# Kernel optimization log

Hardware: AMD Instinct MI355X
Metric: run time of the kernel (lower is better)

The kernel has to match this reference:

```python
import jax, jax.numpy as jnp
import numpy as np

N_NODES = 100000
N_EDGES = 1600000
N_GRAPHS = 512
HID = 192
EPS = 1e-5


def setup_inputs() -> dict:
    key = jax.random.key(0)
    ks = jax.random.split(key, 16)
    x = jax.random.normal(ks[0], (N_NODES, 1), dtype=jnp.float32)
    edge_index = jax.random.randint(ks[1], (2, N_EDGES), 0, N_NODES, dtype=jnp.int64)
    batch = jnp.sort(jax.random.randint(ks[2], (N_NODES,), 0, N_GRAPHS, dtype=jnp.int64))
    def lin(k, fi, fo):
        # torch nn.Linear default init: U(-1/sqrt(fi), 1/sqrt(fi))
        b = 1.0 / np.sqrt(fi)
        return jax.random.uniform(k, (fi, fo), jnp.float32, -b, b)
    return {
        "x": x, "edge_index": edge_index, "batch": batch,
        "W1": lin(ks[3], 1, HID), "b1": jnp.zeros((HID,), jnp.float32),
        "g1": jnp.ones((HID,), jnp.float32), "be1": jnp.zeros((HID,), jnp.float32), "a1": jnp.ones((HID,), jnp.float32),
        "W2": lin(ks[4], HID, HID), "b2": jnp.zeros((HID,), jnp.float32),
        "g2": jnp.ones((HID,), jnp.float32), "be2": jnp.zeros((HID,), jnp.float32), "a2": jnp.ones((HID,), jnp.float32),
        "Wc1": lin(ks[5], HID, HID // 2), "bc1": jax.random.uniform(ks[6], (HID // 2,), jnp.float32, -1/np.sqrt(HID), 1/np.sqrt(HID)),
        "Wc2": lin(ks[7], HID // 2, 4), "bc2": jax.random.uniform(ks[8], (4,), jnp.float32, -1/np.sqrt(HID // 2), 1/np.sqrt(HID // 2)),
    }


def gcn_conv(x, W, b, row, col, n):
    # PyG GCNConv: h = xW; add self-loops; norm = d^-1/2[src] * d^-1/2[dst]; scatter-add to dst; + bias
    h = x @ W
    sl = jnp.arange(n, dtype=row.dtype)
    r = jnp.concatenate([row, sl])
    c = jnp.concatenate([col, sl])
    deg = jax.ops.segment_sum(jnp.ones_like(c, dtype=h.dtype), c, num_segments=n)
    dinv = jnp.where(deg > 0, jax.lax.rsqrt(deg), 0.0)
    norm = dinv[r] * dinv[c]                      # [E+N]
    msg = h[r] * norm[:, None]                    # [E+N, HID] dominant gather
    return jax.ops.segment_sum(msg, c, num_segments=n) + b


def graph_norm(x, batch, gamma, beta, alpha, g):
    cnt = jax.ops.segment_sum(jnp.ones((x.shape[0],), x.dtype), batch, num_segments=g)
    cnt = jnp.maximum(cnt, 1.0)[:, None]
    mean = jax.ops.segment_sum(x, batch, num_segments=g) / cnt
    out = x - alpha * mean[batch]
    var = jax.ops.segment_sum(out * out, batch, num_segments=g) / cnt
    out = out * jax.lax.rsqrt(var + EPS)[batch]
    return gamma * out + beta


def reference(x, edge_index, batch, W1, b1, g1, be1, a1, W2, b2, g2, be2, a2, Wc1, bc1, Wc2, bc2):
    n = x.shape[0]
    row, col = edge_index[0], edge_index[1]
    h = gcn_conv(x, W1, b1, row, col, n)
    h = jax.nn.relu(graph_norm(h, batch, g1, be1, a1, N_GRAPHS))
    h = gcn_conv(h, W2, b2, row, col, n)
    h = jax.nn.relu(graph_norm(h, batch, g2, be2, a2, N_GRAPHS))
    # global mean pool (dropout is identity in eval mode)
    cnt = jnp.maximum(jax.ops.segment_sum(jnp.ones((n,), h.dtype), batch, num_segments=N_GRAPHS), 1.0)
    pooled = jax.ops.segment_sum(h, batch, num_segments=N_GRAPHS) / cnt[:, None]
    z = jax.nn.relu(pooled @ Wc1 + bc1)
    return z @ Wc2 + bc2
```

## Files before the change

### kernel.cpp

```cpp
#include <hip/hip_runtime.h>
#include <hip/hip_bf16.h>
#include <hip/hip_fp16.h>

#define N_NODES 100000
#define N_PAD 100032
#define N_EDGES 1600000
#define N_GRAPHS 512
#define HID 192
#define EPSV 1e-5f

using f16x8 = __attribute__((ext_vector_type(8))) _Float16;
using f16x4 = __attribute__((ext_vector_type(4))) _Float16;
using f32x4 = __attribute__((ext_vector_type(4))) float;

__global__ void k_count(const int* __restrict__ col, int* __restrict__ cnt) {
    int e = blockIdx.x * blockDim.x + threadIdx.x;
    if (e < N_EDGES) atomicAdd(&cnt[col[e]], 1);
}

__global__ void k_misc(const float* __restrict__ W2, _Float16* __restrict__ W2h,
                       const int* __restrict__ batch, int* __restrict__ gstart) {
    int id = blockIdx.x * blockDim.x + threadIdx.x;
    if (id < HID * HID) W2h[id] = (_Float16)W2[id];
    int g = id - HID * HID;
    if (g >= 0 && g <= N_GRAPHS) {
        if (g == N_GRAPHS) { gstart[g] = N_NODES; return; }
        int lo = 0, hi = N_NODES;
        while (lo < hi) { int mid = (lo + hi) >> 1; if (batch[mid] < g) lo = mid + 1; else hi = mid; }
        gstart[g] = lo;
    }
}

__global__ void k_scan_partial(const int* __restrict__ cnt, int* __restrict__ bsum) {
    __shared__ int sd[256];
    int base = blockIdx.x * 1024;
    int t = threadIdx.x;
    int s = 0;
    for (int j = 0; j < 4; ++j) {
        int i = base + j * 256 + t;
        if (i < N_NODES) s += cnt[i];
    }
    sd[t] = s; __syncthreads();
    for (int off = 128; off > 0; off >>= 1) {
        if (t < off) sd[t] += sd[t + off];
        __syncthreads();
    }
    if (t == 0) bsum[blockIdx.x] = sd[0];
}

__global__ void k_scan_final(const int* __restrict__ cnt, const int* __restrict__ bsum,
                             int nb, int* __restrict__ row_ptr, int* __restrict__ cursor,
                             float* __restrict__ dinv, const float* __restrict__ x,
                             float* __restrict__ xp) {
    __shared__ int sd[256];
    __shared__ int s_off;
    int bid = blockIdx.x;
    int t = threadIdx.x;
    int part = 0;
    for (int i = t; i < bid; i += 256) part += bsum[i];
    sd[t] = part; __syncthreads();
    for (int off = 128; off > 0; off >>= 1) {
        if (t < off) sd[t] += sd[t + off];
        __syncthreads();
    }
    if (t == 0) s_off = sd[0];
    __syncthreads();
    int base = bid * 1024;
    int idx0 = base + t * 4;
    int c[4]; int tot = 0;
    for (int j = 0; j < 4; ++j) {
        int i = idx0 + j;
        c[j] = (i < N_NODES) ? cnt[i] : 0;
        tot += c[j];
    }
    sd[t] = tot; __syncthreads();
    for (int off = 1; off < 256; off <<= 1) {
        int v = (t >= off) ? sd[t - off] : 0;
        __syncthreads();
        sd[t] += v;
        __syncthreads();
    }
    int excl = sd[t] - tot + s_off;
    for (int j = 0; j < 4; ++j) {
        int i = idx0 + j;
        if (i < N_NODES) {
            row_ptr[i] = excl;
            cursor[i] = excl;
            float dv = rsqrtf((float)(c[j] + 1));
            dinv[i] = dv;
            xp[i] = x[i] * dv;
            excl += c[j];
        }
    }
    if (bid == nb - 1 && t == 255) row_ptr[N_NODES] = excl;
}

#define FILL_WIN 8
#define FILL_RANGE (N_NODES / FILL_WIN)
#define EPR ((N_EDGES + 255) / 256)
__global__ void __launch_bounds__(256) k_fill(const int* __restrict__ row,
                                              const int* __restrict__ col,
                                              int* __restrict__ cursor,
                                              int* __restrict__ csr_src) {
    int w = blockIdx.x & 7;
    int rank = blockIdx.x >> 3;
    int lo = w * FILL_RANGE;
    int hi = (w == FILL_WIN - 1) ? N_NODES : lo + FILL_RANGE;
    int e0 = rank * EPR;
    int e1 = min(e0 + EPR, N_EDGES);
    for (int e = e0 + threadIdx.x; e < e1; e += 256) {
        int c = col[e];
        if (c >= lo && c < hi) {
            int pos = atomicAdd(&cursor[c], 1);
            csr_src[pos] = row[e];
        }
    }
}

__global__ void k_layer1(const float* __restrict__ x, const float* __restrict__ xp,
                         const int* __restrict__ batch,
                         const int* __restrict__ row_ptr, const int* __restrict__ csr_src,
                         const float* __restrict__ dinv, float4* __restrict__ node_info) {
    int v = blockIdx.x * blockDim.x + threadIdx.x;
    if (v >= N_NODES) return;
    int e0 = row_ptr[v], e1 = row_ptr[v + 1];
    float acc = 0.f;
    for (int base = e0; base < e1; base += 16) {
        int src[16]; float xv[16];
#pragma unroll
        for (int j = 0; j < 16; ++j) { int e = base + j; src[j] = csr_src[(e < e1) ? e : e0]; }
#pragma unroll
        for (int j = 0; j < 16; ++j) { xv[j] = xp[src[j]]; }
#pragma unroll
        for (int j = 0; j < 16; ++j) { acc += (base + j < e1) ? xv[j] : 0.f; }
    }
    float dv = dinv[v];
    float u = dv * acc + x[v] * dv * dv;
    node_info[v] = make_float4(u, dv, __int_as_float((int)batch[v]), 0.f);
}

__global__ void __launch_bounds__(192) k_stats_ab(const float4* __restrict__ node_info,
                                                  const int* __restrict__ gstart,
                                                  const float* __restrict__ W1, const float* __restrict__ b1,
                                                  const float* __restrict__ g1, const float* __restrict__ be1,
                                                  const float* __restrict__ a1,
                                                  float* __restrict__ A, float* __restrict__ B) {
    __shared__ float sd[192], sd2[192];
    int g = blockIdx.x, t = threadIdx.x;
    int i0 = gstart[g], i1 = gstart[g + 1];
    float s = 0.f, s2 = 0.f;
    for (int i = i0 + t; i < i1; i += 192) { float u = node_info[i].x; s += u; s2 += u * u; }
    sd[t] = s; sd2[t] = s2; __syncthreads();
    for (int off = 96; off >= 3; off >>= 1) {
        if (t < off) { sd[t] += sd[t + off]; sd2[t] += sd2[t + off]; }
        __syncthreads();
    }
    float sum_u = sd[0] + sd[1] + sd[2];
    float sum_u2 = sd2[0] + sd2[1] + sd2[2];
    float cntf = fmaxf((float)(i1 - i0), 1.f);
    float m = sum_u / cntf;
    float es2 = sum_u2 / cntf;
    int f = t;
    float w = W1[f], bb = b1[f], al = a1[f];
    float c2 = bb * (1.f - al);
    float d = al * m;
    float eud2 = es2 - 2.f * d * m + d * d;
    float var = w * w * eud2 + 2.f * w * c2 * (m - d) + c2 * c2;
    float rs = rsqrtf(var + EPSV);
    float gam = g1[f];
    A[g * HID + f] = gam * rs * w;
    B[g * HID + f] = gam * rs * (c2 - w * d) + be1[f];
}

__global__ void __launch_bounds__(256) k_x1(const float4* __restrict__ node_info,
                                            const float* __restrict__ A,
                                            const float* __restrict__ B,
                                            _Float16* __restrict__ X1p) {
    int wid = threadIdx.x >> 6;
    int lane = threadIdx.x & 63;
    int v = blockIdx.x * 4 + wid;
    if (v >= N_NODES) return;
    float4 ni = node_info[v];
    float u = ni.x, dv = ni.y;
    int g = __float_as_int(ni.z);
    int c4 = (lane < 48 ? lane : 47) * 4;
    float4 Av = *(const float4*)(A + g * HID + c4);
    float4 Bv = *(const float4*)(B + g * HID + c4);
    f16x4 o;
    o[0] = (_Float16)(fmaxf(fmaf(Av.x, u, Bv.x), 0.f) * dv);
    o[1] = (_Float16)(fmaxf(fmaf(Av.y, u, Bv.y), 0.f) * dv);
    o[2] = (_Float16)(fmaxf(fmaf(Av.z, u, Bv.z), 0.f) * dv);
    o[3] = (_Float16)(fmaxf(fmaf(Av.w, u, Bv.w), 0.f) * dv);
    if (lane < 48) *(f16x4*)(X1p + (size_t)v * HID + c4) = o;
}

#define CH 8
__global__ void __launch_bounds__(256) k_conv2(const _Float16* __restrict__ X1p,
                                               const float* __restrict__ dinv,
                                               const int* __restrict__ row_ptr,
                                               const int* __restrict__ csr_src,
                                               _Float16* __restrict__ aggh) {
    int wid = threadIdx.x >> 6;
    int lane = threadIdx.x & 63;
    int v = blockIdx.x * 4 + wid;
    if (v >= N_NODES) return;
    unsigned c8 = (unsigned)(lane < 48 ? lane : 47) * 8u;
    const char* Xb = (const char*)X1p;
    float dv = dinv[v];
    f16x4 sv = *(const f16x4*)(Xb + (unsigned)v * (HID * 2) + c8);
    float a0 = (float)sv[0], a1 = (float)sv[1], a2 = (float)sv[2], a3 = (float)sv[3];
    int e0 = row_ptr[v], e1 = row_ptr[v + 1];
    for (int b = e0; b < e1; b += CH) {
        unsigned off[CH]; float wgt[CH];
#pragma unroll
        for (int j = 0; j < CH; ++j) {
            int e = b + j;
            off[j] = (unsigned)csr_src[(e < e1) ? e : e0] * (unsigned)(HID * 2) + c8;
            wgt[j] = (e < e1) ? 1.f : 0.f;
        }
        f16x4 rv[CH];
#pragma unroll
        for (int j = 0; j < CH; ++j)
            rv[j] = *(const f16x4*)(Xb + off[j]);
#pragma unroll
        for (int j = 0; j < CH; ++j) {
            a0 = fmaf(wgt[j], (float)rv[j][0], a0);
            a1 = fmaf(wgt[j], (float)rv[j][1], a1);
            a2 = fmaf(wgt[j], (float)rv[j][2], a2);
            a3 = fmaf(wgt[j], (float)rv[j][3], a3);
        }
    }
    if (lane < 48) {
        f16x4 o;
        o[0] = (_Float16)(a0 * dv);
        o[1] = (_Float16)(a1 * dv);
        o[2] = (_Float16)(a2 * dv);
        o[3] = (_Float16)(a3 * dv);
        *(f16x4*)((char*)aggh + (unsigned)v * (HID * 2) + c8) = o;
    }
}

#define BM 64
__global__ void __launch_bounds__(256) k_gemm(const _Float16* __restrict__ A,
                                              const _Float16* __restrict__ W,
                                              const float* __restrict__ b2,
                                              const int* __restrict__ batch,
                                              _Float16* __restrict__ H,
                                              float* __restrict__ sums,
                                              float* __restrict__ sumsq) {
    __shared__ _Float16 a_lds[BM * HID];
    __shared__ int bb[BM];
    int t = threadIdx.x;
    int wid = t >> 6, lane = t & 63;
    int row0 = blockIdx.x * BM;
    if (t < BM) { int gr = row0 + t; bb[t] = (gr < N_NODES) ? batch[gr] : -1; }
    const char* Ablk = (const char*)(A + (size_t)row0 * HID);
#pragma unroll
    for (int it = 0; it < 6; ++it) {
        int bo = (it * 256 + t) * 16;
        int r = bo / 384;
        int swz = bo ^ ((r & 7) << 4);
        *(float4*)((char*)a_lds + swz) = *(const float4*)(Ablk + bo);
    }
    int n0 = wid * 48;
    int bn = n0 + (lane & 15);
    int bk0 = (lane >> 4) << 3;
    f16x8 bfr[6][3];
#pragma unroll
    for (int kc = 0; kc < 6; ++kc)
#pragma unroll
        for (int nt = 0; nt < 3; ++nt) {
            const _Float16* src = W + (size_t)(kc * 32 + bk0) * HID + bn + nt * 16;
            f16x8 v;
#pragma unroll
            for (int j = 0; j < 8; ++j) v[j] = src[(size_t)j * HID];
            bfr[kc][nt] = v;
        }
    __syncthreads();
    f32x4 acc[4][3];
#pragma unroll
    for (int mt = 0; mt < 4; ++mt)
#pragma unroll
        for (int nt = 0; nt < 3; ++nt) acc[mt][nt] = (f32x4){0.f, 0.f, 0.f, 0.f};
    int ar = lane & 15;
#pragma unroll
    for (int mt = 0; mt < 4; ++mt) {
        int r = mt * 16 + ar;
        int rbase = r * 384;
        int sw = (r & 7) << 4;
#pragma unroll
        for (int kc = 0; kc < 6; ++kc) {
            int bo = (rbase + (kc * 32 + bk0) * 2) ^ sw;
            f16x8 a = *(const f16x8*)((const char*)a_lds + bo);
            acc[mt][0] = __builtin_amdgcn_mfma_f32_16x16x32_f16(a, bfr[kc][0], acc[mt][0], 0, 0, 0);
            acc[mt][1] = __builtin_amdgcn_mfma_f32_16x16x32_f16(a, bfr[kc][1], acc[mt][1], 0, 0, 0);
            acc[mt][2] = __builtin_amdgcn_mfma_f32_16x16x32_f16(a, bfr[kc][2], acc[mt][2], 0, 0, 0);
        }
    }
    int cn = lane & 15;
    int rb = (lane >> 4) * 4;
    float bias[3];
#pragma unroll
    for (int nt = 0; nt < 3; ++nt) bias[nt] = b2[n0 + nt * 16 + cn];
    int gA = bb[0];
    int lastv = min(BM, N_NODES - row0) - 1;
    int gB = bb[lastv];
    float sA[3] = {0.f,0.f,0.f}, qA[3] = {0.f,0.f,0.f};
    float sB[3] = {0.f,0.f,0.f}, qB[3] = {0.f,0.f,0.f};
#pragma unroll
    for (int mt = 0; mt < 4; ++mt)
#pragma unroll
        for (int r = 0; r < 4; ++r) {
            int ridx = mt * 16 + rb + r;
            int grow = row0 + ridx;
            if (grow < N_NODES) {
                int gi = bb[ridx];
                _Float16* o = H + (size_t)grow * HID;
#pragma unroll
                for (int nt = 0; nt < 3; ++nt) {
                    float val = acc[mt][nt][r] + bias[nt];
                    o[n0 + nt * 16 + cn] = (_Float16)val;
                    if (gi == gA) { sA[nt] += val; qA[nt] += val * val; }
                    else          { sB[nt] += val; qB[nt] += val * val; }
                }
            }
        }
#pragma unroll
    for (int nt = 0; nt < 3; ++nt) {
        sA[nt] += __shfl_xor(sA[nt], 16); sA[nt] += __shfl_xor(sA[nt], 32);
        qA[nt] += __shfl_xor(qA[nt], 16); qA[nt] += __shfl_xor(qA[nt], 32);
        sB[nt] += __shfl_xor(sB[nt], 16); sB[nt] += __shfl_xor(sB[nt], 32);
        qB[nt] += __shfl_xor(qB[nt], 16); qB[nt] += __shfl_xor(qB[nt], 32);
    }
    if (lane < 16) {
#pragma unroll
        for (int nt = 0; nt < 3; ++nt) {
            int colf = n0 + nt * 16 + cn;
            atomicAdd(&sums[gA * HID + colf], sA[nt]);
            atomicAdd(&sumsq[gA * HID + colf], qA[nt]);
            if (gB != gA) {
                atomicAdd(&sums[gB * HID + colf], sB[nt]);
                atomicAdd(&sumsq[gB * HID + colf], qB[nt]);
            }
        }
    }
}

__global__ void __launch_bounds__(192) k_pool(const _Float16* __restrict__ h,
                                              const int* __restrict__ batch,
                                              const int* __restrict__ gstart,
                                              const float* __restrict__ sums,
                                              const float* __restrict__ sumsq,
                                              const float* __restrict__ g2,
                                              const float* __restrict__ be2,
                                              const float* __restrict__ a2,
                                              float* __restrict__ pooled) {
    int f = threadIdx.x;
    int r0 = blockIdx.x * 64;
    int r1 = min(r0 + 64, N_NODES);
    float al = a2[f], gam = g2[f], bet = be2[f];
    int g = batch[r0];
    float Cg, Dg;
    auto cd = [&](int gg) {
        float cntf = fmaxf((float)(gstart[gg + 1] - gstart[gg]), 1.f);
        float mh = sums[gg * HID + f] / cntf;
        float msq = sumsq[gg * HID + f] / cntf;
        float var = msq - 2.f * al * mh * mh + al * al * mh * mh;
        Cg = gam * rsqrtf(var + EPSV);
        Dg = bet - Cg * al * mh;
    };
    cd(g);
    float s = 0.f;
    int i = r0;
    for (; i + 4 <= r1; i += 4) {
        int g0 = batch[i], g3 = batch[i + 3];
        float v0 = (float)h[(size_t)(i + 0) * HID + f];
        float v1 = (float)h[(size_t)(i + 1) * HID + f];
        float v2 = (float)h[(size_t)(i + 2) * HID + f];
        float v3 = (float)h[(size_t)(i + 3) * HID + f];
        if (g0 == g && g3 == g) {
            s += fmaxf(fmaf(Cg, v0, Dg), 0.f) + fmaxf(fmaf(Cg, v1, Dg), 0.f);
            s += fmaxf(fmaf(Cg, v2, Dg), 0.f) + fmaxf(fmaf(Cg, v3, Dg), 0.f);
        } else {
            float vv[4] = {v0, v1, v2, v3};
            for (int j = 0; j < 4; ++j) {
                int gi = batch[i + j];
                if (gi != g) {
                    atomicAdd(&pooled[g * HID + f], s);
                    s = 0.f; g = gi; cd(g);
                }
                s += fmaxf(fmaf(Cg, vv[j], Dg), 0.f);
            }
        }
    }
    for (; i < r1; ++i) {
        int gi = batch[i];
        float v = (float)h[(size_t)i * HID + f];
        if (gi != g) {
            atomicAdd(&pooled[g * HID + f], s);
            s = 0.f; g = gi; cd(g);
        }
        s += fmaxf(fmaf(Cg, v, Dg), 0.f);
    }
    atomicAdd(&pooled[g * HID + f], s);
}

__global__ void __launch_bounds__(128) k_mlp(const float* __restrict__ pooled,
                                             const int* __restrict__ gstart,
                                             const float* __restrict__ Wc1,
                                             const float* __restrict__ bc1,
                                             const float* __restrict__ Wc2,
                                             const float* __restrict__ bc2,
                                             float* __restrict__ out) {
    __shared__ float p[HID];
    __shared__ float z[96];
    int g = blockIdx.x, t = threadIdx.x;
    float inv = 1.f / fmaxf((float)(gstart[g + 1] - gstart[g]), 1.f);
    for (int i = t; i < HID; i += 128) p[i] = pooled[g * HID + i] * inv;
    __syncthreads();
    if (t < 96) {
        float acc = bc1[t];
        for (int k = 0; k < HID; ++k) acc += p[k] * Wc1[k * 96 + t];
        z[t] = fmaxf(acc, 0.f);
    }
    __syncthreads();
    if (t < 4) {
        float acc = bc2[t];
        for (int j = 0; j < 96; ++j) acc += z[j] * Wc2[j * 4 + t];
        out[g * 4 + t] = acc;
    }
}

extern "C" void kernel_launch(void* const* d_in, const int* in_sizes, int n_in,
                              void* d_out, int out_size, void* d_ws, size_t ws_size,
                              hipStream_t stream) {
    const float* x   = (const float*)d_in[0];
    const int* eidx  = (const int*)d_in[1];
    const int* batch = (const int*)d_in[2];
    const float* W1  = (const float*)d_in[3];
    const float* b1  = (const float*)d_in[4];
    const float* g1  = (const float*)d_in[5];
    const float* be1 = (const float*)d_in[6];
    const float* a1  = (const float*)d_in[7];
    const float* W2  = (const float*)d_in[8];
    const float* b2  = (const float*)d_in[9];
    const float* g2  = (const float*)d_in[10];
    const float* be2 = (const float*)d_in[11];
    const float* a2  = (const float*)d_in[12];
    const float* Wc1 = (const float*)d_in[13];
    const float* bc1 = (const float*)d_in[14];
    const float* Wc2 = (const float*)d_in[15];
    const float* bc2 = (const float*)d_in[16];
    const int* row = eidx;
    const int* col = eidx + N_EDGES;
    float* out = (float*)d_out;

    char* ws = (char*)d_ws;
    size_t off = 0;
    auto alloc = [&](size_t bytes) -> char* {
        char* p = ws + off;
        off = (off + bytes + 255) & ~(size_t)255;
        return p;
    };
    int*   cnt     = (int*)  alloc(N_NODES * 4);
    float* sums2   = (float*)alloc(N_GRAPHS * HID * 4);
    float* sumsq2  = (float*)alloc(N_GRAPHS * HID * 4);
    float* pooled  = (float*)alloc(N_GRAPHS * HID * 4);
    size_t zbytes  = off;
    int*   bsum    = (int*)  alloc(128 * 4);
    int*   row_ptr = (int*)  alloc((N_NODES + 1) * 4);
    int*   cursor  = (int*)  alloc(N_NODES * 4);
    int*   csr_src = (int*)  alloc(N_EDGES * 4);
    float* dinv    = (float*)alloc(N_NODES * 4);
    float* xp      = (float*)alloc(N_NODES * 4);
    float4* node_info = (float4*)alloc((size_t)N_NODES * 16);
    float* Atab    = (float*)alloc(N_GRAPHS * HID * 4);
    float* Btab    = (float*)alloc(N_GRAPHS * HID * 4);
    int*   gstart  = (int*)  alloc((N_GRAPHS + 1) * 4);
    _Float16* X1p  = (_Float16*)alloc((size_t)N_NODES * HID * 2);
    _Float16* aggh = (_Float16*)alloc((size_t)N_PAD * HID * 2);
    _Float16* h2   = (_Float16*)alloc((size_t)N_NODES * HID * 2);
    _Float16* W2h  = (_Float16*)alloc((size_t)HID * HID * 2);

    hipMemsetAsync(ws, 0, zbytes, stream);
    k_misc<<<(HID * HID + N_GRAPHS + 1 + 255) / 256, 256, 0, stream>>>(W2, W2h, batch, gstart);
    k_count<<<(N_EDGES + 255) / 256, 256, 0, stream>>>(col, cnt);
    int PB = (N_NODES + 1023) / 1024;
    k_scan_partial<<<PB, 256, 0, stream>>>(cnt, bsum);
    k_scan_final<<<PB, 256, 0, stream>>>(cnt, bsum, PB, row_ptr, cursor, dinv, x, xp);
    k_fill<<<2048, 256, 0, stream>>>(row, col, cursor, csr_src);
    k_layer1<<<(N_NODES + 255) / 256, 256, 0, stream>>>(x, xp, batch, row_ptr, csr_src, dinv, node_info);
    k_stats_ab<<<N_GRAPHS, 192, 0, stream>>>(node_info, gstart, W1, b1, g1, be1, a1, Atab, Btab);
    k_x1<<<(N_NODES + 3) / 4, 256, 0, stream>>>(node_info, Atab, Btab, X1p);
    k_conv2<<<(N_NODES + 3) / 4, 256, 0, stream>>>(X1p, dinv, row_ptr, csr_src, aggh);
    k_gemm<<<(N_NODES + BM - 1) / BM, 256, 0, stream>>>(aggh, W2h, b2, batch, h2, sums2, sumsq2);
    int SB = (N_NODES + 63) / 64;
    k_pool<<<SB, 192, 0, stream>>>(h2, batch, gstart, sums2, sumsq2, g2, be2, a2, pooled);
    k_mlp<<<N_GRAPHS, 128, 0, stream>>>(pooled, gstart, Wc1, bc1, Wc2, bc2, out);
}
```

Measured before the change: 337.0 us.

## Fuse misc into count, vectorise edge reads, fold layer-1 stats into aggregation

Merges the weight-conversion and graph-start search into the edge-count kernel and reads edge indices as int4 in the count and fill kernels. The per-graph sum of u and u² is now built inside the layer-1 aggregation through wave reductions and atomics, so the per-graph stats kernel becomes a small elementwise A/B kernel. W2 is stored transposed so the GEMM loads B fragments as single vector loads instead of strided scalar loads. This removes launches and a pass over node_info, at the cost of float atomics whose summation order is no longer fixed.

Result: slower. 365.8 us (+8.6%).

```diff
diff --git a/kernel.cpp b/kernel.cpp
--- a/kernel.cpp
+++ b/kernel.cpp
@@ -13,21 +13,32 @@
 using f16x4 = __attribute__((ext_vector_type(4))) _Float16;
 using f32x4 = __attribute__((ext_vector_type(4))) float;
 
-__global__ void k_count(const int* __restrict__ col, int* __restrict__ cnt) {
-    int e = blockIdx.x * blockDim.x + threadIdx.x;
-    if (e < N_EDGES) atomicAdd(&cnt[col[e]], 1);
-}
-
-__global__ void k_misc(const float* __restrict__ W2, _Float16* __restrict__ W2h,
-                       const int* __restrict__ batch, int* __restrict__ gstart) {
+#define NQ4 (N_EDGES / 4)
+
+__global__ void k_count(const int4* __restrict__ col4, int* __restrict__ cnt,
+                        const float* __restrict__ W2, _Float16* __restrict__ W2ht,
+                        const int* __restrict__ batch, int* __restrict__ gstart) {
     int id = blockIdx.x * blockDim.x + threadIdx.x;
-    if (id < HID * HID) W2h[id] = (_Float16)W2[id];
-    int g = id - HID * HID;
-    if (g >= 0 && g <= N_GRAPHS) {
-        if (g == N_GRAPHS) { gstart[g] = N_NODES; return; }
-        int lo = 0, hi = N_NODES;
-        while (lo < hi) { int mid = (lo + hi) >> 1; if (batch[mid] < g) lo = mid + 1; else hi = mid; }
-        gstart[g] = lo;
+    if (id < HID * HID) {
+        int k = id / HID, n = id % HID;
+        W2ht[n * HID + k] = (_Float16)W2[id];
+    } else {
+        int g = id - HID * HID;
+        if (g >= 0 && g <= N_GRAPHS) {
+            if (g == N_GRAPHS) gstart[g] = N_NODES;
+            else {
+                int lo = 0, hi = N_NODES;
+                while (lo < hi) { int mid = (lo + hi) >> 1; if (batch[mid] < g) lo = mid + 1; else hi = mid; }
+                gstart[g] = lo;
+            }
+        }
+    }
+    if (id < NQ4) {
+        int4 c = col4[id];
+        atomicAdd(&cnt[c.x], 1);
+        atomicAdd(&cnt[c.y], 1);
+        atomicAdd(&cnt[c.z], 1);
+        atomicAdd(&cnt[c.w], 1);
     }
 }
 
@@ -97,33 +108,36 @@
 
 #define FILL_WIN 8
 #define FILL_RANGE (N_NODES / FILL_WIN)
-#define EPR ((N_EDGES + 255) / 256)
-__global__ void __launch_bounds__(256) k_fill(const int* __restrict__ row,
-                                              const int* __restrict__ col,
+#define QPR ((NQ4 + 255) / 256)
+__global__ void __launch_bounds__(256) k_fill(const int4* __restrict__ row4,
+                                              const int4* __restrict__ col4,
                                               int* __restrict__ cursor,
                                               int* __restrict__ csr_src) {
     int w = blockIdx.x & 7;
     int rank = blockIdx.x >> 3;
     int lo = w * FILL_RANGE;
     int hi = (w == FILL_WIN - 1) ? N_NODES : lo + FILL_RANGE;
-    int e0 = rank * EPR;
-    int e1 = min(e0 + EPR, N_EDGES);
-    for (int e = e0 + threadIdx.x; e < e1; e += 256) {
-        int c = col[e];
-        if (c >= lo && c < hi) {
-            int pos = atomicAdd(&cursor[c], 1);
-            csr_src[pos] = row[e];
-        }
+    int q0 = rank * QPR;
+    int q1 = min(q0 + QPR, NQ4);
+    for (int q = q0 + threadIdx.x; q < q1; q += 256) {
+        int4 c = col4[q];
+        int4 r = row4[q];
+        if (c.x >= lo && c.x < hi) csr_src[atomicAdd(&cursor[c.x], 1)] = r.x;
+        if (c.y >= lo && c.y < hi) csr_src[atomicAdd(&cursor[c.y], 1)] = r.y;
+        if (c.z >= lo && c.z < hi) csr_src[atomicAdd(&cursor[c.z], 1)] = r.z;
+        if (c.w >= lo && c.w < hi) csr_src[atomicAdd(&cursor[c.w], 1)] = r.w;
     }
 }
 
 __global__ void k_layer1(const float* __restrict__ x, const float* __restrict__ xp,
                          const int* __restrict__ batch,
                          const int* __restrict__ row_ptr, const int* __restrict__ csr_src,
-                         const float* __restrict__ dinv, float4* __restrict__ node_info) {
+                         const float* __restrict__ dinv, float4* __restrict__ node_info,
+                         float* __restrict__ sum_u, float* __restrict__ sum_u2) {
     int v = blockIdx.x * blockDim.x + threadIdx.x;
-    if (v >= N_NODES) return;
-    int e0 = row_ptr[v], e1 = row_ptr[v + 1];
+    bool valid = v < N_NODES;
+    int vc = valid ? v : N_NODES - 1;
+    int e0 = row_ptr[vc], e1 = row_ptr[vc + 1];
     float acc = 0.f;
     for (int base = e0; base < e1; base += 16) {
         int src[16]; float xv[16];
@@ -134,33 +148,39 @@
 #pragma unroll
         for (int j = 0; j < 16; ++j) { acc += (base + j < e1) ? xv[j] : 0.f; }
     }
-    float dv = dinv[v];
-    float u = dv * acc + x[v] * dv * dv;
-    node_info[v] = make_float4(u, dv, __int_as_float((int)batch[v]), 0.f);
-}
-
-__global__ void __launch_bounds__(192) k_stats_ab(const float4* __restrict__ node_info,
-                                                  const int* __restrict__ gstart,
-                                                  const float* __restrict__ W1, const float* __restrict__ b1,
-                                                  const float* __restrict__ g1, const float* __restrict__ be1,
-                                                  const float* __restrict__ a1,
-                                                  float* __restrict__ A, float* __restrict__ B) {
-    __shared__ float sd[192], sd2[192];
-    int g = blockIdx.x, t = threadIdx.x;
-    int i0 = gstart[g], i1 = gstart[g + 1];
-    float s = 0.f, s2 = 0.f;
-    for (int i = i0 + t; i < i1; i += 192) { float u = node_info[i].x; s += u; s2 += u * u; }
-    sd[t] = s; sd2[t] = s2; __syncthreads();
-    for (int off = 96; off >= 3; off >>= 1) {
-        if (t < off) { sd[t] += sd[t + off]; sd2[t] += sd2[t + off]; }
-        __syncthreads();
-    }
-    float sum_u = sd[0] + sd[1] + sd[2];
-    float sum_u2 = sd2[0] + sd2[1] + sd2[2];
-    float cntf = fmaxf((float)(i1 - i0), 1.f);
-    float m = sum_u / cntf;
-    float es2 = sum_u2 / cntf;
-    int f = t;
+    float dv = dinv[vc];
+    float u = dv * acc + x[vc] * dv * dv;
+    int g = batch[vc];
+    if (valid) node_info[v] = make_float4(u, dv, __int_as_float(g), 0.f);
+    float uu = valid ? u : 0.f;
+    int g0 = __shfl(g, 0);
+    bool uni = (__ballot(g == g0) == ~0ull);
+    if (uni) {
+        float s = uu, s2 = uu * uu;
+#pragma unroll
+        for (int off = 32; off; off >>= 1) { s += __shfl_down(s, off); s2 += __shfl_down(s2, off); }
+        if ((threadIdx.x & 63) == 0) {
+            atomicAdd(&sum_u[g0], s);
+            atomicAdd(&sum_u2[g0], s2);
+        }
+    } else {
+        atomicAdd(&sum_u[g], uu);
+        atomicAdd(&sum_u2[g], uu * uu);
+    }
+}
+
+__global__ void k_ab(const float* __restrict__ sum_u, const float* __restrict__ sum_u2,
+                     const int* __restrict__ gstart,
+                     const float* __restrict__ W1, const float* __restrict__ b1,
+                     const float* __restrict__ g1, const float* __restrict__ be1,
+                     const float* __restrict__ a1,
+                     float* __restrict__ A, float* __restrict__ B) {
+    int id = blockIdx.x * blockDim.x + threadIdx.x;
+    if (id >= N_GRAPHS * HID) return;
+    int g = id / HID, f = id % HID;
+    float cntf = fmaxf((float)(gstart[g + 1] - gstart[g]), 1.f);
+    float m = sum_u[g] / cntf;
+    float es2 = sum_u2[g] / cntf;
     float w = W1[f], bb = b1[f], al = a1[f];
     float c2 = bb * (1.f - al);
     float d = al * m;
@@ -168,8 +188,8 @@
     float var = w * w * eud2 + 2.f * w * c2 * (m - d) + c2 * c2;
     float rs = rsqrtf(var + EPSV);
     float gam = g1[f];
-    A[g * HID + f] = gam * rs * w;
-    B[g * HID + f] = gam * rs * (c2 - w * d) + be1[f];
+    A[id] = gam * rs * w;
+    B[id] = gam * rs * (c2 - w * d) + be1[f];
 }
 
 __global__ void __launch_bounds__(256) k_x1(const float4* __restrict__ node_info,
@@ -242,7 +262,7 @@
 
 #define BM 64
 __global__ void __launch_bounds__(256) k_gemm(const _Float16* __restrict__ A,
-                                              const _Float16* __restrict__ W,
+                                              const _Float16* __restrict__ Wt,
                                               const float* __restrict__ b2,
                                               const int* __restrict__ batch,
                                               _Float16* __restrict__ H,
@@ -269,13 +289,8 @@
 #pragma unroll
     for (int kc = 0; kc < 6; ++kc)
 #pragma unroll
-        for (int nt = 0; nt < 3; ++nt) {
-            const _Float16* src = W + (size_t)(kc * 32 + bk0) * HID + bn + nt * 16;
-            f16x8 v;
-#pragma unroll
-            for (int j = 0; j < 8; ++j) v[j] = src[(size_t)j * HID];
-            bfr[kc][nt] = v;
-        }
+        for (int nt = 0; nt < 3; ++nt)
+            bfr[kc][nt] = *(const f16x8*)(Wt + (size_t)(bn + nt * 16) * HID + kc * 32 + bk0);
     __syncthreads();
     f32x4 acc[4][3];
 #pragma unroll
@@ -466,6 +481,8 @@
     float* sums2   = (float*)alloc(N_GRAPHS * HID * 4);
     float* sumsq2  = (float*)alloc(N_GRAPHS * HID * 4);
     float* pooled  = (float*)alloc(N_GRAPHS * HID * 4);
+    float* sum_u   = (float*)alloc(N_GRAPHS * 4);
+    float* sum_u2  = (float*)alloc(N_GRAPHS * 4);
     size_t zbytes  = off;
     int*   bsum    = (int*)  alloc(128 * 4);
     int*   row_ptr = (int*)  alloc((N_NODES + 1) * 4);
@@ -480,20 +497,22 @@
     _Float16* X1p  = (_Float16*)alloc((size_t)N_NODES * HID * 2);
     _Float16* aggh = (_Float16*)alloc((size_t)N_PAD * HID * 2);
     _Float16* h2   = (_Float16*)alloc((size_t)N_NODES * HID * 2);
-    _Float16* W2h  = (_Float16*)alloc((size_t)HID * HID * 2);
+    _Float16* W2ht = (_Float16*)alloc((size_t)HID * HID * 2);
 
     hipMemsetAsync(ws, 0, zbytes, stream);
-    k_misc<<<(HID * HID + N_GRAPHS + 1 + 255) / 256, 256, 0, stream>>>(W2, W2h, batch, gstart);
-    k_count<<<(N_EDGES + 255) / 256, 256, 0, stream>>>(col, cnt);
+    int CB = (NQ4 + 255) / 256;
+    k_count<<<CB, 256, 0, stream>>>((const int4*)col, cnt, W2, W2ht, batch, gstart);
     int PB = (N_NODES + 1023) / 1024;
     k_scan_partial<<<PB, 256, 0, stream>>>(cnt, bsum);
     k_scan_final<<<PB, 256, 0, stream>>>(cnt, bsum, PB, row_ptr, cursor, dinv, x, xp);
-    k_fill<<<2048, 256, 0, stream>>>(row, col, cursor, csr_src);
-    k_layer1<<<(N_NODES + 255) / 256, 256, 0, stream>>>(x, xp, batch, row_ptr, csr_src, dinv, node_info);
-    k_stats_ab<<<N_GRAPHS, 192, 0, stream>>>(node_info, gstart, W1, b1, g1, be1, a1, Atab, Btab);
+    k_fill<<<2048, 256, 0, stream>>>((const int4*)row, (const int4*)col, cursor, csr_src);
+    k_layer1<<<(N_NODES + 255) / 256, 256, 0, stream>>>(x, xp, batch, row_ptr, csr_src, dinv,
+                                                        node_info, sum_u, sum_u2);
+    k_ab<<<(N_GRAPHS * HID + 255) / 256, 256, 0, stream>>>(sum_u, sum_u2, gstart,
+                                                           W1, b1, g1, be1, a1, Atab, Btab);
     k_x1<<<(N_NODES + 3) / 4, 256, 0, stream>>>(node_info, Atab, Btab, X1p);
     k_conv2<<<(N_NODES + 3) / 4, 256, 0, stream>>>(X1p, dinv, row_ptr, csr_src, aggh);
-    k_gemm<<<(N_NODES + BM - 1) / BM, 256, 0, stream>>>(aggh, W2h, b2, batch, h2, sums2, sumsq2);
+    k_gemm<<<(N_NODES + BM - 1) / BM, 256, 0, stream>>>(aggh, W2ht, b2, batch, h2, sums2, sumsq2);
     int SB = (N_NODES + 63) / 64;
     k_pool<<<SB, 192, 0, stream>>>(h2, batch, gstart, sums2, sumsq2, g2, be2, a2, pooled);
     k_mlp<<<N_GRAPHS, 128, 0, stream>>>(pooled, gstart, Wc1, bc1, Wc2, bc2, out);
```
